# Performance work log

Hardware: AMD Instinct MI355X
Metric: run time of the kernel (lower is better)

Reference implementation:

```python
import jax, jax.numpy as jnp
import numpy as np

C = 1.0          # ball curvature c (manifold k = -c)
RC = 1.0         # sqrt(c)
PROJ_EPS = 4e-3  # geoopt float32 projection eps
NUM_HEADS = 16
B, S, D = 2, 1024, 1024


def _project(x):
    # clip points back inside the Poincare ball
    maxnorm = (1.0 - PROJ_EPS) / RC
    norm = jnp.maximum(jnp.linalg.norm(x, axis=-1, keepdims=True), 1e-15)
    return jnp.where(norm > maxnorm, x / norm * maxnorm, x)


def _poincare_linear(x, z, r, out_split):
    # Unidirectional Poincare MLR (Shimizu et al., HNN++) followed by exp-map back to the ball.
    # x: [..., din]; z: [din, dout]; r: [dout]
    z_norm = jnp.maximum(jnp.linalg.norm(z, axis=0, keepdims=True), 1e-15)  # [1, dout]
    z_unit = z / z_norm
    drcr = 2.0 * RC * r                                    # [dout]
    rcx = RC * x
    cx2 = jnp.sum(rcx * rcx, axis=-1, keepdims=True)       # [..., 1]
    w = 2.0 * (z_norm / RC) * jnp.arcsinh(
        (2.0 * (rcx @ z_unit) * jnp.cosh(drcr) - (1.0 + cx2) * jnp.sinh(drcr))
        / jnp.maximum(1.0 - cx2, 1e-15))
    y = jnp.sinh(RC * w) / RC
    y = y.reshape(y.shape[:-1] + (out_split, y.shape[-1] // out_split))  # [..., H, dh]
    y = _project(y)
    y = y / (1.0 + jnp.sqrt(1.0 + C * jnp.sum(y * y, axis=-1, keepdims=True)))
    return _project(y)


def _dist_matmul(x, y):
    # Pairwise Poincare distance via matmul. x: [..., n, d], y: [..., d, m].
    # dist = (1/sqrt(c)) * arccosh(1 + 2c||x-y||^2 / ((1-c||x||^2)(1-c||y||^2)))
    xy = jnp.matmul(x, y)
    x2 = jnp.sum(x * x, axis=-1, keepdims=True)           # [..., n, 1]
    y2 = jnp.sum(y * y, axis=-2, keepdims=True)           # [..., 1, m]
    num = jnp.maximum(x2 - 2.0 * xy + y2, 1e-15)          # ||x - y||^2
    den = jnp.maximum((1.0 - C * x2) * (1.0 - C * y2), 1e-15)
    return (1.0 / RC) * jnp.arccosh(1.0 + 2.0 * C * num / den)


def _weighted_midpoint_bmm(xs, weights):
    # Weighted Mobius gyromidpoint. xs: [..., n, d], weights: [..., m, n] -> [..., m, d]
    x2 = jnp.sum(xs * xs, axis=-1, keepdims=True)
    gamma = 2.0 / jnp.maximum(1.0 - C * x2, 1e-15)        # conformal factor lambda_x
    denom = jnp.matmul(jnp.abs(weights), gamma - 1.0)     # [..., m, 1]
    nomin = jnp.matmul(weights, gamma * xs)               # [..., m, d]
    two_mean = nomin / jnp.maximum(denom, 1e-10)
    sq = jnp.sum(two_mean * two_mean, axis=-1, keepdims=True)
    a_mean = two_mean / (1.0 + jnp.sqrt(jnp.maximum(1.0 - C * sq, 1e-15)))
    return _project(a_mean)


def setup_inputs() -> dict:
    key = jax.random.key(0)
    ks = jax.random.split(key, 4)
    # points must lie inside the unit ball: ||x|| ~ 0.02*sqrt(D) ~ 0.64
    hidden_states = 0.02 * jax.random.normal(ks[0], (B, S, D), dtype=jnp.float32)
    attention_mask = jnp.zeros((B, 1, 1, S), dtype=jnp.float32)
    scale = 1.0 / np.sqrt(D).astype(np.float32)
    qz = scale * jax.random.normal(ks[1], (D, D), dtype=jnp.float32)
    kz = scale * jax.random.normal(ks[2], (D, D), dtype=jnp.float32)
    vz = scale * jax.random.normal(ks[3], (D, D), dtype=jnp.float32)
    qr = jnp.zeros((D,), jnp.float32)
    kr = jnp.zeros((D,), jnp.float32)
    vr = jnp.zeros((D,), jnp.float32)
    return {"hidden_states": hidden_states, "attention_mask": attention_mask,
            "qz": qz, "qr": qr, "kz": kz, "kr": kr, "vz": vz, "vr": vr}


def reference(hidden_states, attention_mask, qz, qr, kz, kr, vz, vr):
    # self-attention path (encoder_hidden_states is None), eval mode (dropout p=0)
    q = _poincare_linear(hidden_states, qz, qr, NUM_HEADS).transpose(0, 2, 1, 3)  # [B,H,S,dh]
    k = _poincare_linear(hidden_states, kz, kr, NUM_HEADS).transpose(0, 2, 1, 3)
    v = _poincare_linear(hidden_states, vz, vr, NUM_HEADS).transpose(0, 2, 1, 3)
    scores = -_dist_matmul(q, jnp.swapaxes(k, -1, -2)) + attention_mask          # [B,H,S,S]
    probs = jax.nn.softmax(scores, axis=-1)
    ctx = _weighted_midpoint_bmm(v, probs)                                       # [B,H,S,dh]
    b, h, s, dh = ctx.shape
    return ctx.transpose(0, 2, 1, 3).reshape(b, s, h * dh)
```

## Files before the change

kernel.cpp:

```cpp
#include <hip/hip_runtime.h>
#include <math.h>

#define BB 2
#define SS 1024
#define DD 1024
#define NH 16
#define DH 64
#define MAXN 0.996f

typedef __attribute__((ext_vector_type(8))) short bf16x8;
typedef __attribute__((ext_vector_type(4))) float f32x4;

__device__ __forceinline__ float xor_sum16(float v){
  v += __shfl_xor(v, 1, 64);
  v += __shfl_xor(v, 2, 64);
  v += __shfl_xor(v, 4, 64);
  v += __shfl_xor(v, 8, 64);
  return v;
}

__device__ __forceinline__ unsigned short f2bf(float x){
  unsigned u = __builtin_bit_cast(unsigned, x);
  unsigned r = u + 0x7FFFu + ((u >> 16) & 1u);
  return (unsigned short)(r >> 16);
}
__device__ __forceinline__ float bf2f(unsigned short b){
  unsigned u = ((unsigned)b) << 16;
  return __builtin_bit_cast(float, u);
}

__device__ __forceinline__ void async_copy16(const unsigned short* g, unsigned short* s){
  __builtin_amdgcn_global_load_lds(
      (const __attribute__((address_space(1))) unsigned int*)g,
      (__attribute__((address_space(3))) unsigned int*)s,
      16, 0, 0);
}

__global__ __launch_bounds__(256) void prep_kernel(
    const float* __restrict__ hs,
    const float* __restrict__ zq, const float* __restrict__ zk, const float* __restrict__ zv,
    float* __restrict__ cx2, float* __restrict__ partial,
    unsigned short* __restrict__ Xhi, unsigned short* __restrict__ Xlo,
    unsigned short* __restrict__ ZThi, unsigned short* __restrict__ ZTlo)
{
  __shared__ unsigned shbuf[64 * 69];
  __shared__ float csred[4][64];
  const int bid = blockIdx.x;
  const int tid = threadIdx.x;

  if (bid < 1024) {
    const int b = bid;
    const size_t g0 = (size_t)b * 2048 + (size_t)tid * 8;
    float acc = 0.0f;
    #pragma unroll
    for (int h = 0; h < 2; ++h) {
      float4 v = *(const float4*)(hs + g0 + 4 * h);
      float a[4] = {v.x, v.y, v.z, v.w};
      ushort4 hv, lv;
      unsigned short* hp = (unsigned short*)&hv;
      unsigned short* lp = (unsigned short*)&lv;
      #pragma unroll
      for (int j = 0; j < 4; ++j) {
        acc = fmaf(a[j], a[j], acc);
        unsigned short hi = f2bf(a[j]);
        hp[j] = hi;
        lp[j] = f2bf(a[j] - bf2f(hi));
      }
      *(ushort4*)(Xhi + g0 + 4 * h) = hv;
      *(ushort4*)(Xlo + g0 + 4 * h) = lv;
    }
    #pragma unroll
    for (int m = 1; m < 64; m <<= 1) acc += __shfl_xor(acc, m, 64);
    float* red = (float*)shbuf;
    const int wave = tid >> 6, lane = tid & 63;
    if (lane == 0) red[wave] = acc;
    __syncthreads();
    if (tid == 0)   cx2[2 * b]     = red[0] + red[1];
    if (tid == 128) cx2[2 * b + 1] = red[2] + red[3];
  } else {
    const int b2 = bid - 1024;
    const int kt = b2 & 15, nt = (b2 >> 4) & 15, mat = b2 >> 8;
    const float* z = (mat == 0) ? zq : ((mat == 1) ? zk : zv);
    const int wave = tid >> 6, lane = tid & 63;
    unsigned (*T)[69] = (unsigned(*)[69])shbuf;
    float cs[4] = {0.f, 0.f, 0.f, 0.f};
    #pragma unroll
    for (int i = 0; i < 4; ++i) {
      const int g = tid + 256 * i;
      const int kr = g >> 4, nc = (g & 15) * 4;
      float4 v = *(const float4*)(z + (size_t)(kt * 64 + kr) * DD + nt * 64 + nc);
      float a[4] = {v.x, v.y, v.z, v.w};
      #pragma unroll
      for (int j = 0; j < 4; ++j) {
        cs[j] = fmaf(a[j], a[j], cs[j]);
        unsigned short hi = f2bf(a[j]);
        unsigned short lo = f2bf(a[j] - bf2f(hi));
        T[kr][nc + j] = ((unsigned)lo << 16) | (unsigned)hi;
      }
    }
    #pragma unroll
    for (int j = 0; j < 4; ++j) {
      cs[j] += __shfl_xor(cs[j], 16, 64);
      cs[j] += __shfl_xor(cs[j], 32, 64);
    }
    if (lane < 16) {
      #pragma unroll
      for (int j = 0; j < 4; ++j) csred[wave][lane * 4 + j] = cs[j];
    }
    __syncthreads();
    #pragma unroll
    for (int i = 0; i < 4; ++i) {
      const int g = tid + 256 * i;
      const int nr = g >> 4, kc = (g & 15) * 4;
      ushort4 hv, lv;
      unsigned short* hp = (unsigned short*)&hv;
      unsigned short* lp = (unsigned short*)&lv;
      #pragma unroll
      for (int j = 0; j < 4; ++j) {
        unsigned u = T[kc + j][nr];
        hp[j] = (unsigned short)(u & 0xFFFFu);
        lp[j] = (unsigned short)(u >> 16);
      }
      const size_t ob = ((size_t)mat * DD + nt * 64 + nr) * DD + kt * 64 + kc;
      *(ushort4*)(ZThi + ob) = hv;
      *(ushort4*)(ZTlo + ob) = lv;
    }
    if (tid < 64) {
      float s = csred[0][tid] + csred[1][tid] + csred[2][tid] + csred[3][tid];
      partial[kt * 3072 + mat * DD + nt * 64 + tid] = s;
    }
  }
}

__global__ __launch_bounds__(256) void colstats_finalize_kernel(
    const float* __restrict__ partial,
    const float* __restrict__ rq, const float* __restrict__ rk, const float* __restrict__ rv,
    float* __restrict__ acol, float* __restrict__ bcol, float* __restrict__ scol)
{
  const int col = blockIdx.x * 256 + threadIdx.x;
  float s = 0.f;
  #pragma unroll
  for (int rc = 0; rc < 16; ++rc) s += partial[rc * 3072 + col];
  const int m = col >> 10, c = col & 1023;
  const float* r = (m == 0) ? rq : ((m == 1) ? rk : rv);
  const float n = fmaxf(sqrtf(s), 1e-15f);
  const float rr = 2.0f * r[c];
  acol[col] = 2.0f * coshf(rr) / n;
  bcol[col] = sinhf(rr);
  scol[col] = 2.0f * n;
}

__global__ __launch_bounds__(256, 2) void gemm_mfma_kernel(
    const unsigned short* __restrict__ Xhi, const unsigned short* __restrict__ Xlo,
    const unsigned short* __restrict__ ZThi, const unsigned short* __restrict__ ZTlo,
    const float* __restrict__ acol, const float* __restrict__ bcol, const float* __restrict__ scol,
    const float* __restrict__ cx2,
    unsigned short* __restrict__ Qhi, unsigned short* __restrict__ Qlo,
    unsigned short* __restrict__ Khi, unsigned short* __restrict__ Klo,
    unsigned short* __restrict__ GThi, unsigned short* __restrict__ GTlo,
    float* __restrict__ q2, float* __restrict__ k2, float* __restrict__ gm1)
{
  __shared__ __align__(16) unsigned char shmem[66560];
  unsigned short* Sbuf = (unsigned short*)shmem;

  const int mat = blockIdx.z;
  float* Stat = (mat == 0) ? q2 : ((mat == 1) ? k2 : gm1);
  unsigned short* Bh = (mat == 0) ? Qhi : Khi;
  unsigned short* Bl = (mat == 0) ? Qlo : Klo;

  const int n0 = blockIdx.x * 128;
  const int m0 = blockIdx.y * 128;
  const int tid = threadIdx.x;
  const int wave = tid >> 6, lane = tid & 63;
  const int tx = lane & 15, quad = lane >> 4;
  const int wrow = wave >> 1;
  const int wcol = wave & 1;

  const int l4r = lane >> 2;
  const int l4c = 8 * (((lane & 3) - (l4r >> 1)) & 3);
  const unsigned short* abase =
      (wave == 0) ? Xhi : (wave == 1) ? Xlo : (wave == 2) ? ZThi : ZTlo;
  const size_t rowbase = (wave < 2) ? (size_t)m0 : (size_t)(mat * DD + n0);
  const unsigned short* P[8];
  #pragma unroll
  for (int i = 0; i < 8; ++i)
    P[i] = abase + (rowbase + i * 16 + l4r) * DD + l4c;
  const int ldsw = 4096 * wave;

  const int koff = 8 * ((quad + (tx >> 1)) & 3);

  const f32x4 z4 = {0.f, 0.f, 0.f, 0.f};
  f32x4 acc[4][4];
  #pragma unroll
  for (int mb = 0; mb < 4; ++mb)
    #pragma unroll
    for (int nb = 0; nb < 4; ++nb) acc[mb][nb] = z4;

  #pragma unroll
  for (int i = 0; i < 8; ++i) {
    async_copy16(P[i], Sbuf + ldsw + 512 * i);
    P[i] += 32;
  }

  for (int kt = 0; kt < 32; ++kt) {
    __syncthreads();
    if (kt < 31) {
      unsigned short* Bn = Sbuf + 16384 * ((kt + 1) & 1);
      #pragma unroll
      for (int i = 0; i < 8; ++i) {
        async_copy16(P[i], Bn + ldsw + 512 * i);
        P[i] += 32;
      }
    }
    const unsigned short* Bc = Sbuf + 16384 * (kt & 1);

    bf16x8 a_h[4], a_l[4];
    #pragma unroll
    for (int mb = 0; mb < 4; ++mb) {
      const int ar = 64 * wrow + 16 * mb + tx;
      a_h[mb] = *(const bf16x8*)&Bc[ar * 32 + koff];
      a_l[mb] = *(const bf16x8*)&Bc[4096 + ar * 32 + koff];
    }
    #pragma unroll
    for (int nb = 0; nb < 4; ++nb) {
      const int br = 64 * wcol + 16 * nb + tx;
      bf16x8 b_h = *(const bf16x8*)&Bc[8192 + br * 32 + koff];
      bf16x8 b_l = *(const bf16x8*)&Bc[12288 + br * 32 + koff];
      #pragma unroll
      for (int mb = 0; mb < 4; ++mb)
        acc[mb][nb] = __builtin_amdgcn_mfma_f32_16x16x32_bf16(a_h[mb], b_h, acc[mb][nb], 0, 0, 0);
      #pragma unroll
      for (int mb = 0; mb < 4; ++mb)
        acc[mb][nb] = __builtin_amdgcn_mfma_f32_16x16x32_bf16(a_h[mb], b_l, acc[mb][nb], 0, 0, 0);
      #pragma unroll
      for (int mb = 0; mb < 4; ++mb)
        acc[mb][nb] = __builtin_amdgcn_mfma_f32_16x16x32_bf16(a_l[mb], b_h, acc[mb][nb], 0, 0, 0);
    }
  }

  const int head = blockIdx.x * 2 + wcol;
  unsigned* Tr = (unsigned*)shmem;
  if (mat == 2) __syncthreads();

  #pragma unroll
  for (int mb = 0; mb < 4; ++mb) {
    #pragma unroll
    for (int r = 0; r < 4; ++r) {
      const int sl = 64 * wrow + 16 * mb + 4 * quad + r;
      const int row = m0 + sl;
      const float c2 = cx2[row];
      const float inv = 1.0f / fmaxf(1.0f - c2, 1e-15f);
      const float onec = 1.0f + c2;
      float yv[4];
      #pragma unroll
      for (int nb = 0; nb < 4; ++nb) {
        const float accv = acc[mb][nb][r];
        const int col = mat * DD + n0 + 64 * wcol + 16 * nb + tx;
        const float u = fmaf(accv, acol[col], -(onec * bcol[col])) * inv;
        const float a = fabsf(u);
        const float t = a + sqrtf(fmaf(a, a, 1.0f));
        const float p = __builtin_amdgcn_exp2f(scol[col] * __builtin_amdgcn_logf(t));
        float y = 0.5f * (p - __builtin_amdgcn_rcpf(p));
        yv[nb] = copysignf(y, u);
      }
      const int b = row >> 10, s = row & 1023;
      float n2 = 0.f;
      #pragma unroll
      for (int j = 0; j < 4; ++j) n2 = fmaf(yv[j], yv[j], n2);
      n2 = xor_sum16(n2);
      float n = fmaxf(sqrtf(n2), 1e-15f);
      float s1 = (n > MAXN) ? (MAXN / n) : 1.0f;
      n2 = n2 * s1 * s1;
      float f = 1.0f / (1.0f + sqrtf(1.0f + n2));
      float fs = s1 * f;
      n2 = n2 * f * f;
      float nb2 = fmaxf(sqrtf(n2), 1e-15f);
      float s2f = (nb2 > MAXN) ? (MAXN / nb2) : 1.0f;
      fs *= s2f;
      n2 = n2 * s2f * s2f;

      const size_t bh = (size_t)(b * NH + head);
      const size_t outbase = (bh * SS + s) * DH;
      if (mat == 2) {
        const float gamma = 2.0f / fmaxf(1.0f - n2, 1e-15f);
        #pragma unroll
        for (int j = 0; j < 4; ++j) {
          const float v = yv[j] * fs * gamma;
          const unsigned short hi = f2bf(v);
          const unsigned short lo = f2bf(v - bf2f(hi));
          Tr[(wcol * 128 + sl) * 65 + 16 * j + tx] = ((unsigned)lo << 16) | (unsigned)hi;
        }
        if (tx == 0) Stat[bh * SS + s] = gamma - 1.0f;
      } else {
        #pragma unroll
        for (int j = 0; j < 4; ++j) {
          const float v = yv[j] * fs;
          const unsigned short hi = f2bf(v);
          const unsigned short lo = f2bf(v - bf2f(hi));
          Bh[outbase + 16 * j + tx] = hi;
          Bl[outbase + 16 * j + tx] = lo;
        }
        if (tx == 0) Stat[bh * SS + s] = n2;
      }
    }
  }

  if (mat == 2) {
    __syncthreads();
    const int bb = m0 >> 10, sbase = m0 & 1023;
    #pragma unroll
    for (int i = 0; i < 4; ++i) {
      const int task = tid + 256 * i;
      const int rowid = task >> 3;
      const int hh = rowid >> 6, dh = rowid & 63;
      const int sc = (task & 7) * 16;
      unsigned short hbuf[16] __attribute__((aligned(16)));
      unsigned short lbuf[16] __attribute__((aligned(16)));
      #pragma unroll
      for (int s = 0; s < 16; ++s) {
        unsigned u = Tr[(hh * 128 + sc + s) * 65 + dh];
        hbuf[s] = (unsigned short)(u & 0xFFFFu);
        lbuf[s] = (unsigned short)(u >> 16);
      }
      const int hg = blockIdx.x * 2 + hh;
      const size_t ob = (((size_t)(bb * NH + hg)) * DH + dh) * SS + sbase + sc;
      *(uint4*)(GThi + ob)     = *(uint4*)&hbuf[0];
      *(uint4*)(GThi + ob + 8) = *(uint4*)&hbuf[8];
      *(uint4*)(GTlo + ob)     = *(uint4*)&lbuf[0];
      *(uint4*)(GTlo + ob + 8) = *(uint4*)&lbuf[8];
    }
  }
}

__global__ __launch_bounds__(256) void flash_attn_kernel(
    const unsigned short* __restrict__ Qhi, const unsigned short* __restrict__ Qlo,
    const unsigned short* __restrict__ Khi, const unsigned short* __restrict__ Klo,
    const unsigned short* __restrict__ GThi, const unsigned short* __restrict__ GTlo,
    const float* __restrict__ q2a, const float* __restrict__ k2a, const float* __restrict__ gm1a,
    const float* __restrict__ mask, float* __restrict__ out)
{
  constexpr int LDK = 88;
  __shared__ unsigned short Ks_hi[64 * LDK];
  __shared__ unsigned short Ks_lo[64 * LDK];
  __shared__ unsigned short Gs_hi[64 * LDK];
  __shared__ unsigned short Gs_lo[64 * LDK];
  __shared__ unsigned short Ps_hi[64 * LDK];
  __shared__ unsigned short Ps_lo[64 * LDK];
  __shared__ float k2s[64], ik2s[64], gm1s[64], ems[64];

  const int h = blockIdx.x, qt = blockIdx.y, b = blockIdx.z;
  const int bh = b * NH + h;
  const int tid = threadIdx.x;
  const int wave = tid >> 6, lane = tid & 63;
  const int tx = lane & 15, quad = lane >> 4;
  const int r0 = qt * 64;

  bf16x8 qa_h[2], qa_l[2];
  {
    const size_t qoff = ((size_t)bh * SS + r0 + 16 * wave + tx) * DH;
    #pragma unroll
    for (int kc = 0; kc < 2; ++kc) {
      qa_h[kc] = *(const bf16x8*)(Qhi + qoff + 32 * kc + 8 * quad);
      qa_l[kc] = *(const bf16x8*)(Qlo + qoff + 32 * kc + 8 * quad);
    }
  }
  float q2r[4], iq2[4];
  #pragma unroll
  for (int r = 0; r < 4; ++r) {
    q2r[r] = q2a[(size_t)bh * SS + r0 + 16 * wave + 4 * quad + r];
    iq2[r] = 2.0f / fmaxf(1.0f - q2r[r], 1e-15f);
  }

  const f32x4 zero4 = {0.f, 0.f, 0.f, 0.f};
  f32x4 oacc[4] = {zero4, zero4, zero4, zero4};
  float dden[4] = {0.f, 0.f, 0.f, 0.f};

  const int c0 = tid, c1 = tid + 256;
  const int sr0 = c0 >> 3, sc0 = (c0 & 7) * 8;
  const int sr1 = c1 >> 3, sc1 = (c1 & 7) * 8;

  const size_t kbase = (size_t)bh * SS * DH;
  const size_t gbase = (size_t)bh * DH * SS;

  uint4 pk_h0 = *(const uint4*)(Khi + kbase + (size_t)sr0 * DH + sc0);
  uint4 pk_h1 = *(const uint4*)(Khi + kbase + (size_t)sr1 * DH + sc1);
  uint4 pk_l0 = *(const uint4*)(Klo + kbase + (size_t)sr0 * DH + sc0);
  uint4 pk_l1 = *(const uint4*)(Klo + kbase + (size_t)sr1 * DH + sc1);
  uint4 pg_h0 = *(const uint4*)(GThi + gbase + (size_t)sr0 * SS + sc0);
  uint4 pg_h1 = *(const uint4*)(GThi + gbase + (size_t)sr1 * SS + sc1);
  uint4 pg_l0 = *(const uint4*)(GTlo + gbase + (size_t)sr0 * SS + sc0);
  uint4 pg_l1 = *(const uint4*)(GTlo + gbase + (size_t)sr1 * SS + sc1);
  float p_k2 = 0.f, p_gm1 = 0.f, p_ms = 0.f;
  if (tid < 64) {
    p_k2  = k2a[(size_t)bh * SS + tid];
    p_gm1 = gm1a[(size_t)bh * SS + tid];
    p_ms  = mask[(size_t)b * SS + tid];
  }

  for (int kt = 0; kt < 16; ++kt) {
    __syncthreads();
    *(uint4*)&Ks_hi[sr0 * LDK + sc0] = pk_h0;
    *(uint4*)&Ks_hi[sr1 * LDK + sc1] = pk_h1;
    *(uint4*)&Ks_lo[sr0 * LDK + sc0] = pk_l0;
    *(uint4*)&Ks_lo[sr1 * LDK + sc1] = pk_l1;
    *(uint4*)&Gs_hi[sr0 * LDK + sc0] = pg_h0;
    *(uint4*)&Gs_hi[sr1 * LDK + sc1] = pg_h1;
    *(uint4*)&Gs_lo[sr0 * LDK + sc0] = pg_l0;
    *(uint4*)&Gs_lo[sr1 * LDK + sc1] = pg_l1;
    if (tid < 64) {
      k2s[tid]  = p_k2;
      ik2s[tid] = 1.0f / fmaxf(1.0f - p_k2, 1e-15f);
      gm1s[tid] = p_gm1;
      ems[tid]  = __expf(p_ms);
    }
    __syncthreads();
    if (kt < 15) {
      const int t1 = (kt + 1) * 64;
      const size_t kb_ = kbase + (size_t)t1 * DH;
      const size_t gb_ = gbase + t1;
      pk_h0 = *(const uint4*)(Khi + kb_ + (size_t)sr0 * DH + sc0);
      pk_h1 = *(const uint4*)(Khi + kb_ + (size_t)sr1 * DH + sc1);
      pk_l0 = *(const uint4*)(Klo + kb_ + (size_t)sr0 * DH + sc0);
      pk_l1 = *(const uint4*)(Klo + kb_ + (size_t)sr1 * DH + sc1);
      pg_h0 = *(const uint4*)(GThi + gb_ + (size_t)sr0 * SS + sc0);
      pg_h1 = *(const uint4*)(GThi + gb_ + (size_t)sr1 * SS + sc1);
      pg_l0 = *(const uint4*)(GTlo + gb_ + (size_t)sr0 * SS + sc0);
      pg_l1 = *(const uint4*)(GTlo + gb_ + (size_t)sr1 * SS + sc1);
      if (tid < 64) {
        p_k2  = k2a[(size_t)bh * SS + t1 + tid];
        p_gm1 = gm1a[(size_t)bh * SS + t1 + tid];
        p_ms  = mask[(size_t)b * SS + t1 + tid];
      }
    }

    f32x4 sacc[4] = {zero4, zero4, zero4, zero4};
    #pragma unroll
    for (int kc = 0; kc < 2; ++kc) {
      const int ko = 32 * kc + 8 * quad;
      #pragma unroll
      for (int nb = 0; nb < 4; ++nb) {
        bf16x8 kh = *(const bf16x8*)&Ks_hi[(16 * nb + tx) * LDK + ko];
        bf16x8 kl = *(const bf16x8*)&Ks_lo[(16 * nb + tx) * LDK + ko];
        sacc[nb] = __builtin_amdgcn_mfma_f32_16x16x32_bf16(qa_h[kc], kh, sacc[nb], 0, 0, 0);
        sacc[nb] = __builtin_amdgcn_mfma_f32_16x16x32_bf16(qa_h[kc], kl, sacc[nb], 0, 0, 0);
        sacc[nb] = __builtin_amdgcn_mfma_f32_16x16x32_bf16(qa_l[kc], kh, sacc[nb], 0, 0, 0);
      }
    }

    float pb[4][4];
    #pragma unroll
    for (int nb = 0; nb < 4; ++nb) {
      const int key = 16 * nb + tx;
      const float k2v = k2s[key], ikv = ik2s[key], emv = ems[key], gmv = gm1s[key];
      #pragma unroll
      for (int r = 0; r < 4; ++r) {
        float sv = sacc[nb][r];
        float num = fmaxf(fmaf(-2.0f, sv, q2r[r] + k2v), 1e-15f);
        float e = num * iq2[r] * ikv;
        float g = fmaf(e, e, e + e);
        float z = 1.0f + e + __builtin_amdgcn_sqrtf(g);
        float w = emv * __builtin_amdgcn_rcpf(z);
        pb[r][nb] = w;
        dden[r] = fmaf(w, gmv, dden[r]);
      }
    }

    #pragma unroll
    for (int r = 0; r < 4; ++r) {
      const int prow = 16 * wave + 4 * quad + r;
      #pragma unroll
      for (int nb = 0; nb < 4; ++nb) {
        float w = pb[r][nb];
        unsigned short hi = f2bf(w);
        unsigned short lo = f2bf(w - bf2f(hi));
        Ps_hi[prow * LDK + 16 * nb + tx] = hi;
        Ps_lo[prow * LDK + 16 * nb + tx] = lo;
      }
    }
    #pragma unroll
    for (int kc = 0; kc < 2; ++kc) {
      const int ko = 32 * kc + 8 * quad;
      bf16x8 ph = *(const bf16x8*)&Ps_hi[(16 * wave + tx) * LDK + ko];
      bf16x8 pl = *(const bf16x8*)&Ps_lo[(16 * wave + tx) * LDK + ko];
      #pragma unroll
      for (int nb = 0; nb < 4; ++nb) {
        bf16x8 gh = *(const bf16x8*)&Gs_hi[(16 * nb + tx) * LDK + ko];
        bf16x8 gl = *(const bf16x8*)&Gs_lo[(16 * nb + tx) * LDK + ko];
        oacc[nb] = __builtin_amdgcn_mfma_f32_16x16x32_bf16(ph, gh, oacc[nb], 0, 0, 0);
        oacc[nb] = __builtin_amdgcn_mfma_f32_16x16x32_bf16(ph, gl, oacc[nb], 0, 0, 0);
        oacc[nb] = __builtin_amdgcn_mfma_f32_16x16x32_bf16(pl, gh, oacc[nb], 0, 0, 0);
      }
    }
  }

  #pragma unroll
  for (int r = 0; r < 4; ++r) {
    float d = fmaxf(xor_sum16(dden[r]), 1e-10f);
    float invd = 1.0f / d;
    float tm[4]; float sq = 0.f;
    #pragma unroll
    for (int nb = 0; nb < 4; ++nb) { tm[nb] = oacc[nb][r] * invd; sq = fmaf(tm[nb], tm[nb], sq); }
    sq = xor_sum16(sq);
    const float f = 1.0f / (1.0f + sqrtf(fmaxf(1.0f - sq, 1e-15f)));
    const float n2 = sq * f * f;
    const float n = fmaxf(sqrtf(n2), 1e-15f);
    const float s2 = (n > MAXN) ? (MAXN / n) : 1.0f;
    const float fs = f * s2;
    const int qrow = r0 + 16 * wave + 4 * quad + r;
    #pragma unroll
    for (int nb = 0; nb < 4; ++nb)
      out[((size_t)(b * SS + qrow)) * DD + h * DH + 16 * nb + tx] = tm[nb] * fs;
  }
}

extern "C" void kernel_launch(void* const* d_in, const int* in_sizes, int n_in,
                              void* d_out, int out_size, void* d_ws, size_t ws_size,
                              hipStream_t stream) {
  const float* hs   = (const float*)d_in[0];
  const float* mask = (const float*)d_in[1];
  const float* qz   = (const float*)d_in[2];
  const float* qr   = (const float*)d_in[3];
  const float* kz   = (const float*)d_in[4];
  const float* kr   = (const float*)d_in[5];
  const float* vz   = (const float*)d_in[6];
  const float* vr   = (const float*)d_in[7];
  float* out = (float*)d_out;

  float* ws = (float*)d_ws;
  const size_t nQKV = (size_t)BB * NH * SS * DH;
  const size_t nStat = (size_t)BB * NH * SS;

  float* q2  = ws;
  float* k2  = q2 + nStat;
  float* gm1 = k2 + nStat;
  float* acol = gm1 + nStat;
  float* bcol = acol + 3 * DD;
  float* scol = bcol + 3 * DD;
  float* cx2 = scol + 3 * DD;
  float* partial = cx2 + 2048;

  unsigned short* sb   = (unsigned short*)(partial + 16 * 3072);
  unsigned short* Qhi  = sb;
  unsigned short* Qlo  = Qhi + nQKV;
  unsigned short* Khi  = Qlo + nQKV;
  unsigned short* Klo  = Khi + nQKV;
  unsigned short* GThi = Klo + nQKV;
  unsigned short* GTlo = GThi + nQKV;
  unsigned short* Xhi  = GTlo + nQKV;
  unsigned short* Xlo  = Xhi + nQKV;
  unsigned short* ZThi = Xlo + nQKV;
  unsigned short* ZTlo = ZThi + 3 * (size_t)DD * DD;

  prep_kernel<<<dim3(1792), 256, 0, stream>>>(
      hs, qz, kz, vz, cx2, partial, Xhi, Xlo, ZThi, ZTlo);
  colstats_finalize_kernel<<<dim3(12), 256, 0, stream>>>(
      partial, qr, kr, vr, acol, bcol, scol);
  gemm_mfma_kernel<<<dim3(8, 16, 3), 256, 0, stream>>>(
      Xhi, Xlo, ZThi, ZTlo, acol, bcol, scol, cx2,
      Qhi, Qlo, Khi, Klo, GThi, GTlo, q2, k2, gm1);
  flash_attn_kernel<<<dim3(NH, 16, BB), 256, 0, stream>>>(
      Qhi, Qlo, Khi, Klo, GThi, GTlo, q2, k2, gm1, mask, out);
}
```

Baseline: 200.9 us.

## Double-buffer K/G tiles with async global-to-LDS copies and swizzled layout

The attention loop now uses 32-key tiles held in two LDS buffers. Each wave issues direct async 16-byte copies of one operand array (K hi, K lo, G hi or G lo) into the buffer for the next tile while the current one is computed. This takes the register staging and the second barrier per iteration out of the loop. The padded LDS rows are replaced by an XOR-style rotated layout to avoid bank conflicts, and the per-key scalars are double-buffered too. In exchange the loop runs twice as many iterations with smaller MFMA batches per barrier, and correctness depends on the async copies finishing before the barrier.

```diff
diff --git a/kernel.cpp b/kernel.cpp
--- a/kernel.cpp
+++ b/kernel.cpp
@@ -339,14 +339,13 @@
     const float* __restrict__ q2a, const float* __restrict__ k2a, const float* __restrict__ gm1a,
     const float* __restrict__ mask, float* __restrict__ out)
 {
-  constexpr int LDK = 88;
-  __shared__ unsigned short Ks_hi[64 * LDK];
-  __shared__ unsigned short Ks_lo[64 * LDK];
-  __shared__ unsigned short Gs_hi[64 * LDK];
-  __shared__ unsigned short Gs_lo[64 * LDK];
-  __shared__ unsigned short Ps_hi[64 * LDK];
-  __shared__ unsigned short Ps_lo[64 * LDK];
-  __shared__ float k2s[64], ik2s[64], gm1s[64], ems[64];
+  __shared__ unsigned short Ksh[2][2048];
+  __shared__ unsigned short Ksl[2][2048];
+  __shared__ unsigned short Gsh[2][2048];
+  __shared__ unsigned short Gsl[2][2048];
+  __shared__ unsigned short Psh[64 * 40];
+  __shared__ unsigned short Psl[64 * 40];
+  __shared__ float k2s[2][32], ik2s[2][32], gm1s[2][32], ems[2][32];
 
   const int h = blockIdx.x, qt = blockIdx.y, b = blockIdx.z;
   const int bh = b * NH + h;
@@ -375,83 +374,93 @@
   f32x4 oacc[4] = {zero4, zero4, zero4, zero4};
   float dden[4] = {0.f, 0.f, 0.f, 0.f};
 
-  const int c0 = tid, c1 = tid + 256;
-  const int sr0 = c0 >> 3, sc0 = (c0 & 7) * 8;
-  const int sr1 = c1 >> 3, sc1 = (c1 & 7) * 8;
-
   const size_t kbase = (size_t)bh * SS * DH;
   const size_t gbase = (size_t)bh * DH * SS;
 
-  uint4 pk_h0 = *(const uint4*)(Khi + kbase + (size_t)sr0 * DH + sc0);
-  uint4 pk_h1 = *(const uint4*)(Khi + kbase + (size_t)sr1 * DH + sc1);
-  uint4 pk_l0 = *(const uint4*)(Klo + kbase + (size_t)sr0 * DH + sc0);
-  uint4 pk_l1 = *(const uint4*)(Klo + kbase + (size_t)sr1 * DH + sc1);
-  uint4 pg_h0 = *(const uint4*)(GThi + gbase + (size_t)sr0 * SS + sc0);
-  uint4 pg_h1 = *(const uint4*)(GThi + gbase + (size_t)sr1 * SS + sc1);
-  uint4 pg_l0 = *(const uint4*)(GTlo + gbase + (size_t)sr0 * SS + sc0);
-  uint4 pg_l1 = *(const uint4*)(GTlo + gbase + (size_t)sr1 * SS + sc1);
-  float p_k2 = 0.f, p_gm1 = 0.f, p_ms = 0.f;
-  if (tid < 64) {
-    p_k2  = k2a[(size_t)bh * SS + tid];
-    p_gm1 = gm1a[(size_t)bh * SS + tid];
-    p_ms  = mask[(size_t)b * SS + tid];
-  }
-
-  for (int kt = 0; kt < 16; ++kt) {
+  const unsigned short* sArr =
+      (wave == 0) ? Khi : (wave == 1) ? Klo : (wave == 2) ? GThi : GTlo;
+  const unsigned short* sBase = sArr + ((wave < 2) ? kbase : gbase);
+  const int tAdv = (wave < 2) ? 32 * DH : 32;
+  int srcoff[4];
+  if (wave < 2) {
+    #pragma unroll
+    for (int i = 0; i < 4; ++i) {
+      const int r = 8 * i + (lane >> 3);
+      srcoff[i] = r * DH + 8 * (((lane & 7) - r) & 7);
+    }
+  } else {
+    #pragma unroll
+    for (int i = 0; i < 4; ++i) {
+      const int r = 16 * i + (lane >> 2);
+      srcoff[i] = r * SS + 8 * (((lane & 3) - r) & 3);
+    }
+  }
+  unsigned short* ldsDst[2];
+  ldsDst[0] = (wave == 0) ? Ksh[0] : (wave == 1) ? Ksl[0] : (wave == 2) ? Gsh[0] : Gsl[0];
+  ldsDst[1] = (wave == 0) ? Ksh[1] : (wave == 1) ? Ksl[1] : (wave == 2) ? Gsh[1] : Gsl[1];
+
+  float s_k2 = 0.f, s_gm1 = 0.f, s_ms = 0.f;
+
+  {
+    const unsigned short* s = sBase;
+    #pragma unroll
+    for (int i = 0; i < 4; ++i) async_copy16(s + srcoff[i], ldsDst[0] + i * 512);
+  }
+  if (tid < 32) {
+    s_k2  = k2a[(size_t)bh * SS + tid];
+    s_gm1 = gm1a[(size_t)bh * SS + tid];
+    s_ms  = mask[(size_t)b * SS + tid];
+    k2s[0][tid]  = s_k2;
+    ik2s[0][tid] = 1.0f / fmaxf(1.0f - s_k2, 1e-15f);
+    gm1s[0][tid] = s_gm1;
+    ems[0][tid]  = __expf(s_ms);
+    s_k2  = k2a[(size_t)bh * SS + 32 + tid];
+    s_gm1 = gm1a[(size_t)bh * SS + 32 + tid];
+    s_ms  = mask[(size_t)b * SS + 32 + tid];
+  }
+
+  for (int kt = 0; kt < 32; ++kt) {
     __syncthreads();
-    *(uint4*)&Ks_hi[sr0 * LDK + sc0] = pk_h0;
-    *(uint4*)&Ks_hi[sr1 * LDK + sc1] = pk_h1;
-    *(uint4*)&Ks_lo[sr0 * LDK + sc0] = pk_l0;
-    *(uint4*)&Ks_lo[sr1 * LDK + sc1] = pk_l1;
-    *(uint4*)&Gs_hi[sr0 * LDK + sc0] = pg_h0;
-    *(uint4*)&Gs_hi[sr1 * LDK + sc1] = pg_h1;
-    *(uint4*)&Gs_lo[sr0 * LDK + sc0] = pg_l0;
-    *(uint4*)&Gs_lo[sr1 * LDK + sc1] = pg_l1;
-    if (tid < 64) {
-      k2s[tid]  = p_k2;
-      ik2s[tid] = 1.0f / fmaxf(1.0f - p_k2, 1e-15f);
-      gm1s[tid] = p_gm1;
-      ems[tid]  = __expf(p_ms);
-    }
-    __syncthreads();
-    if (kt < 15) {
-      const int t1 = (kt + 1) * 64;
-      const size_t kb_ = kbase + (size_t)t1 * DH;
-      const size_t gb_ = gbase + t1;
-      pk_h0 = *(const uint4*)(Khi + kb_ + (size_t)sr0 * DH + sc0);
-      pk_h1 = *(const uint4*)(Khi + kb_ + (size_t)sr1 * DH + sc1);
-      pk_l0 = *(const uint4*)(Klo + kb_ + (size_t)sr0 * DH + sc0);
-      pk_l1 = *(const uint4*)(Klo + kb_ + (size_t)sr1 * DH + sc1);
-      pg_h0 = *(const uint4*)(GThi + gb_ + (size_t)sr0 * SS + sc0);
-      pg_h1 = *(const uint4*)(GThi + gb_ + (size_t)sr1 * SS + sc1);
-      pg_l0 = *(const uint4*)(GTlo + gb_ + (size_t)sr0 * SS + sc0);
-      pg_l1 = *(const uint4*)(GTlo + gb_ + (size_t)sr1 * SS + sc1);
-      if (tid < 64) {
-        p_k2  = k2a[(size_t)bh * SS + t1 + tid];
-        p_gm1 = gm1a[(size_t)bh * SS + t1 + tid];
-        p_ms  = mask[(size_t)b * SS + t1 + tid];
-      }
-    }
-
-    f32x4 sacc[4] = {zero4, zero4, zero4, zero4};
+    if (kt < 31) {
+      const int nbuf = (kt + 1) & 1;
+      const unsigned short* s = sBase + (size_t)(kt + 1) * tAdv;
+      #pragma unroll
+      for (int i = 0; i < 4; ++i) async_copy16(s + srcoff[i], ldsDst[nbuf] + i * 512);
+      if (tid < 32) {
+        k2s[nbuf][tid]  = s_k2;
+        ik2s[nbuf][tid] = 1.0f / fmaxf(1.0f - s_k2, 1e-15f);
+        gm1s[nbuf][tid] = s_gm1;
+        ems[nbuf][tid]  = __expf(s_ms);
+        if (kt < 30) {
+          const int t2 = (kt + 2) * 32;
+          s_k2  = k2a[(size_t)bh * SS + t2 + tid];
+          s_gm1 = gm1a[(size_t)bh * SS + t2 + tid];
+          s_ms  = mask[(size_t)b * SS + t2 + tid];
+        }
+      }
+    }
+    const int cb = kt & 1;
+
+    f32x4 sacc[2] = {zero4, zero4};
     #pragma unroll
     for (int kc = 0; kc < 2; ++kc) {
-      const int ko = 32 * kc + 8 * quad;
-      #pragma unroll
-      for (int nb = 0; nb < 4; ++nb) {
-        bf16x8 kh = *(const bf16x8*)&Ks_hi[(16 * nb + tx) * LDK + ko];
-        bf16x8 kl = *(const bf16x8*)&Ks_lo[(16 * nb + tx) * LDK + ko];
+      #pragma unroll
+      for (int nb = 0; nb < 2; ++nb) {
+        const int row = 16 * nb + tx;
+        const int off = row * 64 + 8 * (((4 * kc + quad) + row) & 7);
+        bf16x8 kh = *(const bf16x8*)&Ksh[cb][off];
+        bf16x8 kl = *(const bf16x8*)&Ksl[cb][off];
         sacc[nb] = __builtin_amdgcn_mfma_f32_16x16x32_bf16(qa_h[kc], kh, sacc[nb], 0, 0, 0);
         sacc[nb] = __builtin_amdgcn_mfma_f32_16x16x32_bf16(qa_h[kc], kl, sacc[nb], 0, 0, 0);
         sacc[nb] = __builtin_amdgcn_mfma_f32_16x16x32_bf16(qa_l[kc], kh, sacc[nb], 0, 0, 0);
       }
     }
 
-    float pb[4][4];
-    #pragma unroll
-    for (int nb = 0; nb < 4; ++nb) {
+    float pb[4][2];
+    #pragma unroll
+    for (int nb = 0; nb < 2; ++nb) {
       const int key = 16 * nb + tx;
-      const float k2v = k2s[key], ikv = ik2s[key], emv = ems[key], gmv = gm1s[key];
+      const float k2v = k2s[cb][key], ikv = ik2s[cb][key], emv = ems[cb][key], gmv = gm1s[cb][key];
       #pragma unroll
       for (int r = 0; r < 4; ++r) {
         float sv = sacc[nb][r];
@@ -469,27 +478,25 @@
     for (int r = 0; r < 4; ++r) {
       const int prow = 16 * wave + 4 * quad + r;
       #pragma unroll
-      for (int nb = 0; nb < 4; ++nb) {
+      for (int nb = 0; nb < 2; ++nb) {
         float w = pb[r][nb];
         unsigned short hi = f2bf(w);
         unsigned short lo = f2bf(w - bf2f(hi));
-        Ps_hi[prow * LDK + 16 * nb + tx] = hi;
-        Ps_lo[prow * LDK + 16 * nb + tx] = lo;
-      }
-    }
-    #pragma unroll
-    for (int kc = 0; kc < 2; ++kc) {
-      const int ko = 32 * kc + 8 * quad;
-      bf16x8 ph = *(const bf16x8*)&Ps_hi[(16 * wave + tx) * LDK + ko];
-      bf16x8 pl = *(const bf16x8*)&Ps_lo[(16 * wave + tx) * LDK + ko];
-      #pragma unroll
-      for (int nb = 0; nb < 4; ++nb) {
-        bf16x8 gh = *(const bf16x8*)&Gs_hi[(16 * nb + tx) * LDK + ko];
-        bf16x8 gl = *(const bf16x8*)&Gs_lo[(16 * nb + tx) * LDK + ko];
-        oacc[nb] = __builtin_amdgcn_mfma_f32_16x16x32_bf16(ph, gh, oacc[nb], 0, 0, 0);
-        oacc[nb] = __builtin_amdgcn_mfma_f32_16x16x32_bf16(ph, gl, oacc[nb], 0, 0, 0);
-        oacc[nb] = __builtin_amdgcn_mfma_f32_16x16x32_bf16(pl, gh, oacc[nb], 0, 0, 0);
-      }
+        Psh[prow * 40 + 16 * nb + tx] = hi;
+        Psl[prow * 40 + 16 * nb + tx] = lo;
+      }
+    }
+    bf16x8 ph = *(const bf16x8*)&Psh[(16 * wave + tx) * 40 + 8 * quad];
+    bf16x8 pl = *(const bf16x8*)&Psl[(16 * wave + tx) * 40 + 8 * quad];
+    #pragma unroll
+    for (int nb = 0; nb < 4; ++nb) {
+      const int row = 16 * nb + tx;
+      const int off = row * 32 + 8 * ((quad + row) & 3);
+      bf16x8 gh = *(const bf16x8*)&Gsh[cb][off];
+      bf16x8 gl = *(const bf16x8*)&Gsl[cb][off];
+      oacc[nb] = __builtin_amdgcn_mfma_f32_16x16x32_bf16(ph, gh, oacc[nb], 0, 0, 0);
+      oacc[nb] = __builtin_amdgcn_mfma_f32_16x16x32_bf16(ph, gl, oacc[nb], 0, 0, 0);
+      oacc[nb] = __builtin_amdgcn_mfma_f32_16x16x32_bf16(pl, gh, oacc[nb], 0, 0, 0);
     }
   }
 
```

Result: no change. 200.2 us (-0.3%).
